# Optimization experiments

Hardware: AMD Instinct MI355X
Metric: run time of the kernel (lower is better)

## Reference

```python
import jax, jax.numpy as jnp
import numpy as np
from jax import lax

B, L, H = 2, 4096, 2048
NH = 16
DK = H // NH  # num_slot = 128 (q/k dim)
C = 64        # chunk size
EPS = 1e-5
N_LAYER = 24


def setup_inputs() -> dict:
    key = jax.random.key(0)
    ks = jax.random.split(key, 7)
    std = 0.02
    return {
        "hidden_states": jax.random.normal(ks[0], (B, L, H), jnp.float32),
        "Wq": jax.random.normal(ks[1], (DK, H), jnp.float32) * std,
        "Wk": jax.random.normal(ks[2], (DK, H), jnp.float32) * std,
        "Wog": jax.random.normal(ks[3], (H, H), jnp.float32) * std,
        "Wig": jax.random.normal(ks[4], (H, H), jnp.float32) * std,
        "Wo": jax.random.normal(ks[5], (H, H), jnp.float32) * (std / np.sqrt(2 * N_LAYER)),
        "g_norm_w": jnp.ones((H,), jnp.float32),
    }


def _gla_chunk(q, k, v, gf):
    # q,k,gf: [b,L,dk]; v: [b,L,dv]. Recurrence: S_t = diag(exp(gf_t)) S_{t-1} + k_t v_t^T; o_t = q_t S_t
    b, Ls, dk = q.shape
    dv = v.shape[-1]
    n = Ls // C
    # [n, b, C, d] so scan iterates over chunks
    qc = q.reshape(b, n, C, dk).transpose(1, 0, 2, 3)
    kc = k.reshape(b, n, C, dk).transpose(1, 0, 2, 3)
    vc = v.reshape(b, n, C, dv).transpose(1, 0, 2, 3)
    gc = gf.reshape(b, n, C, dk).transpose(1, 0, 2, 3)
    Bc = jnp.cumsum(gc, axis=2)  # inclusive within-chunk log-decay

    tril = jnp.tril(jnp.ones((C, C), bool))

    def step(S, inp):
        qh, kh, vh, Bh = inp  # [b,C,dk],[b,C,dk],[b,C,dv],[b,C,dk]
        Blast = Bh[:, -1, :]  # [b,dk]
        # exp(B_i - B_j) <= 1 for j <= i (gf < 0): numerically safe pairwise form
        D = Bh[:, :, None, :] - Bh[:, None, :, :]  # [b,C,C,dk]
        A = jnp.einsum('bid,bjd,bijd->bij', qh, kh, jnp.exp(D))
        A = jnp.where(tril, A, 0.0)
        o_intra = jnp.einsum('bij,bjv->biv', A, vh)
        o_inter = jnp.einsum('bid,bdv->biv', qh * jnp.exp(Bh), S)
        kd = kh * jnp.exp(Blast[:, None, :] - Bh)  # <= 1 scaling, safe
        S_new = S * jnp.exp(Blast)[..., None] + jnp.einsum('bjd,bjv->bdv', kd, vh)
        return S_new, o_intra + o_inter

    S0 = jnp.zeros((b, dk, dv), q.dtype)
    _, o = lax.scan(step, S0, (qc, kc, vc, Bc))  # o: [n,b,C,dv]
    return o.transpose(1, 0, 2, 3).reshape(b, Ls, dv)


def reference(hidden_states, Wq, Wk, Wog, Wig, Wo, g_norm_w):
    x = hidden_states
    q = jax.nn.softmax(x @ Wq.T, axis=-1)        # [b,L,dk]
    k = jax.nn.sigmoid(x @ Wk.T)                 # [b,L,dk]
    v = x                                        # value_dim == hidden_size
    gf = jax.nn.log_sigmoid(-k)                  # per-key-dim log decay, in (-1.32, -0.69)
    o = _gla_chunk(q, k, v, gf)                  # [b,L,H]
    # output gate: og_proj(o) + ig_proj(x), fused RMSNorm + swish gate
    go = o @ Wog.T + x @ Wig.T
    on = o * lax.rsqrt(jnp.mean(o * o, axis=-1, keepdims=True) + EPS) * g_norm_w
    o = on * (go * jax.nn.sigmoid(go))
    return o @ Wo.T
```

## Files before the change

kernel.cpp:

```cpp
#include <hip/hip_runtime.h>
#include <hip/hip_bf16.h>

typedef __hip_bfloat16 bf16;
typedef __bf16 bf16x8 __attribute__((ext_vector_type(8)));
typedef float f32x4 __attribute__((ext_vector_type(4)));

__device__ __forceinline__ void async16(void* lds_base, const void* g) {
  __builtin_amdgcn_global_load_lds(
      (const __attribute__((address_space(1))) void*)g,
      (__attribute__((address_space(3))) void*)lds_base, 16, 0, 0);
}

__global__ void cvt_bf16_kernel(const float* __restrict__ s, bf16* __restrict__ d, int n4) {
  const int i = blockIdx.x * 256 + threadIdx.x;
  if (i >= n4) return;
  const float4 v = ((const float4*)s)[i];
  bf16 h0 = __float2bfloat16(v.x), h1 = __float2bfloat16(v.y);
  bf16 h2 = __float2bfloat16(v.z), h3 = __float2bfloat16(v.w);
  ushort4 o;
  o.x = *(unsigned short*)&h0; o.y = *(unsigned short*)&h1;
  o.z = *(unsigned short*)&h2; o.w = *(unsigned short*)&h3;
  *(ushort4*)((unsigned short*)d + (size_t)i * 4) = o;
}

__global__ __launch_bounds__(256) void convert_x_kernel(
    const float* __restrict__ x, bf16* __restrict__ xb, bf16* __restrict__ xbT) {
  __shared__ float tile[64][65];
  const int b = blockIdx.z;
  const int l0 = blockIdx.x * 64, d0 = blockIdx.y * 64;
  const int t = threadIdx.x;
  const int c = t & 63, r4 = t >> 6;
  const size_t base = ((size_t)b * 4096 + l0) * 2048 + d0;
#pragma unroll
  for (int i = 0; i < 16; ++i) {
    const int row = i * 4 + r4;
    const float v = x[base + (size_t)row * 2048 + c];
    tile[row][c] = v;
    xb[base + (size_t)row * 2048 + c] = __float2bfloat16(v);
  }
  __syncthreads();
  const size_t baseT = ((size_t)b * 2048 + d0) * 4096 + l0;
#pragma unroll
  for (int i = 0; i < 16; ++i) {
    const int dr = i * 4 + r4;
    xbT[baseT + (size_t)dr * 4096 + c] = __float2bfloat16(tile[c][dr]);
  }
}

template <int MODE>
__global__ __launch_bounds__(256, 2) void gemm_bt(
    const bf16* __restrict__ A0, const bf16* __restrict__ B0,
    const bf16* __restrict__ A1, const bf16* __restrict__ B1,
    float* __restrict__ outf, bf16* __restrict__ outb,
    const bf16* __restrict__ o_in, const float* __restrict__ rmsv,
    const float* __restrict__ gnw, int M, int N, int K) {
  __shared__ bf16 lA[128 * 32];
  __shared__ bf16 lB[128 * 32];
  const int tid = threadIdx.x;
  const int lane = tid & 63, wave = tid >> 6;
  const int l15 = lane & 15, l4 = lane >> 4;
  const int bm = blockIdx.x * 128, bn = blockIdx.y * 128;
  const int wm = (wave & 1) * 64, wn = (wave >> 1) * 64;
  const int srow = tid >> 2;
  const int skc = (tid & 3) * 8;

  const f32x4 fz = {0.f, 0.f, 0.f, 0.f};
  f32x4 acc[4][4];
#pragma unroll
  for (int i = 0; i < 4; ++i)
#pragma unroll
    for (int j = 0; j < 4; ++j) acc[i][j] = fz;

  bf16* lAu  = lA + wave * 512;
  bf16* lAu2 = lA + 2048 + wave * 512;
  bf16* lBu  = lB + wave * 512;
  bf16* lBu2 = lB + 2048 + wave * 512;

  const int npass = (MODE == 1) ? 2 : 1;
  for (int pass = 0; pass < npass; ++pass) {
    const bf16* Ap = (pass == 0) ? A0 : A1;
    const bf16* Bp = (pass == 0) ? B0 : B1;
    const bf16* gA0 = Ap + (size_t)(bm + srow) * K + skc;
    const bf16* gA1 = Ap + (size_t)(bm + srow + 64) * K + skc;
    const bf16* gB0 = Bp + (size_t)(bn + srow) * K + skc;
    const bf16* gB1 = Bp + (size_t)(bn + srow + 64) * K + skc;
    for (int k0 = 0; k0 < K; k0 += 32) {
      __syncthreads();
      async16(lAu, gA0 + k0);
      async16(lAu2, gA1 + k0);
      async16(lBu, gB0 + k0);
      async16(lBu2, gB1 + k0);
      __syncthreads();
      bf16x8 af[4], bfv[4];
#pragma unroll
      for (int mt = 0; mt < 4; ++mt)
        af[mt] = *(const bf16x8*)(lA + (wm + mt * 16 + l15) * 32 + l4 * 8);
#pragma unroll
      for (int nt = 0; nt < 4; ++nt)
        bfv[nt] = *(const bf16x8*)(lB + (wn + nt * 16 + l15) * 32 + l4 * 8);
#pragma unroll
      for (int mt = 0; mt < 4; ++mt)
#pragma unroll
        for (int nt = 0; nt < 4; ++nt)
          acc[mt][nt] = __builtin_amdgcn_mfma_f32_16x16x32_bf16(af[mt], bfv[nt], acc[mt][nt], 0, 0, 0);
    }
  }

#pragma unroll
  for (int mt = 0; mt < 4; ++mt)
#pragma unroll
    for (int r = 0; r < 4; ++r) {
      const int gr = bm + wm + mt * 16 + l4 * 4 + r;
#pragma unroll
      for (int nt = 0; nt < 4; ++nt) {
        const int gc = bn + wn + nt * 16 + l15;
        const float v = acc[mt][nt][r];
        if (MODE == 1) {
          const float o = (float)o_in[(size_t)gr * N + gc];
          const float on = o * rmsv[gr] * gnw[gc];
          const float sw = v / (1.f + __expf(-v));
          outb[(size_t)gr * N + gc] = __float2bfloat16(on * sw);
        } else {
          outf[(size_t)gr * N + gc] = v;
        }
      }
    }
}

__global__ __launch_bounds__(64) void qk_post_kernel(
    const float* __restrict__ logits, bf16* __restrict__ qb,
    bf16* __restrict__ kb, float* __restrict__ gfl) {
  const int row = blockIdx.x;
  const int t = threadIdx.x;
  const float* lr = logits + (size_t)row * 256;
  float a0 = lr[t], a1 = lr[t + 64];
  float m = fmaxf(a0, a1);
#pragma unroll
  for (int s = 32; s; s >>= 1) m = fmaxf(m, __shfl_xor(m, s));
  float e0 = __expf(a0 - m), e1 = __expf(a1 - m);
  float sum = e0 + e1;
#pragma unroll
  for (int s = 32; s; s >>= 1) sum += __shfl_xor(sum, s);
  const float inv = 1.f / sum;
  qb[(size_t)row * 128 + t]      = __float2bfloat16(e0 * inv);
  qb[(size_t)row * 128 + t + 64] = __float2bfloat16(e1 * inv);
  float b0 = lr[128 + t], b1 = lr[128 + t + 64];
  float k0 = 1.f / (1.f + __expf(-b0));
  float k1 = 1.f / (1.f + __expf(-b1));
  kb[(size_t)row * 128 + t]      = __float2bfloat16(k0);
  kb[(size_t)row * 128 + t + 64] = __float2bfloat16(k1);
  gfl[(size_t)row * 128 + t]      = -log1pf(__expf(k0));
  gfl[(size_t)row * 128 + t + 64] = -log1pf(__expf(k1));
}

__global__ __launch_bounds__(256, 2) void gla_kernel(
    const bf16* __restrict__ qb, const bf16* __restrict__ kb,
    const float* __restrict__ gfl, const bf16* __restrict__ xbT,
    bf16* __restrict__ ob, float* __restrict__ rmsv) {
  __shared__ bf16 sF1[64][136];
  __shared__ bf16 sF2[128][136];
  __shared__ float sM[128];
  __shared__ float rowsq[64];
  const int tid = threadIdx.x;
  const int lane = tid & 63, wave = tid >> 6;
  const int l15 = lane & 15, l4 = lane >> 4;
  const int chunk = blockIdx.x, b = blockIdx.y;
  const int row0 = b * 4096 + chunk * 64;

  if (tid < 64) rowsq[tid] = 0.f;

  if (tid < 128) {
    float s = 0.f;
    for (int i = 0; i <= 32; ++i) s += gfl[(size_t)(row0 + i) * 128 + tid];
    sM[tid] = s;
  }
  __syncthreads();

  if (tid < 128) {
    const int d = tid;
    const float M = sM[d];
    float bi = 0.f;
    for (int i = 0; i < 64; ++i) {
      bi += gfl[(size_t)(row0 + i) * 128 + d];
      const float q = (float)qb[(size_t)(row0 + i) * 128 + d];
      const float k = (float)kb[(size_t)(row0 + i) * 128 + d];
      sF1[i][d]      = __float2bfloat16(q * __expf(bi - M));
      sF2[64 + i][d] = __float2bfloat16(k * __expf(M - bi));
    }
  } else {
    const int d = tid - 128;
    if (chunk == 0) {
      for (int j = 0; j < 64; ++j) sF2[j][d] = __float2bfloat16(0.f);
    } else {
      const float M = sM[d];
      float bw = 0.f;
      for (int j = 63; j >= 0; --j) {
        const float k = (float)kb[(size_t)(row0 - 64 + j) * 128 + d];
        sF2[j][d] = __float2bfloat16(k * __expf(M - bw));
        bw -= gfl[(size_t)(row0 - 64 + j) * 128 + d];
      }
    }
  }
  __syncthreads();

  const f32x4 fz = {0.f, 0.f, 0.f, 0.f};
  {
    f32x4 sacc[4][2];
#pragma unroll
    for (int mt = 0; mt < 4; ++mt) { sacc[mt][0] = fz; sacc[mt][1] = fz; }
    bf16x8 f1[4][4];
#pragma unroll
    for (int kt = 0; kt < 4; ++kt)
#pragma unroll
      for (int mt = 0; mt < 4; ++mt)
        f1[kt][mt] = *(const bf16x8*)(&sF1[mt * 16 + l15][kt * 32 + l4 * 8]);
#pragma unroll
    for (int nt = 0; nt < 2; ++nt)
#pragma unroll
      for (int kt = 0; kt < 4; ++kt) {
        const bf16x8 f2 = *(const bf16x8*)(&sF2[wave * 32 + nt * 16 + l15][kt * 32 + l4 * 8]);
#pragma unroll
        for (int mt = 0; mt < 4; ++mt)
          sacc[mt][nt] = __builtin_amdgcn_mfma_f32_16x16x32_bf16(f1[kt][mt], f2, sacc[mt][nt], 0, 0, 0);
      }
    __syncthreads();
#pragma unroll
    for (int mt = 0; mt < 4; ++mt)
#pragma unroll
      for (int nt = 0; nt < 2; ++nt)
#pragma unroll
        for (int r = 0; r < 4; ++r) {
          const int i = mt * 16 + l4 * 4 + r;
          const int jw = wave * 32 + nt * 16 + l15;
          const bool ok = (jw < 64) || (jw - 64 <= i);
          sF1[i][jw] = __float2bfloat16(ok ? sacc[mt][nt][r] : 0.f);
        }
    __syncthreads();
  }

  bf16x8 av[4][4];
#pragma unroll
  for (int kt = 0; kt < 4; ++kt)
#pragma unroll
    for (int mt = 0; mt < 4; ++mt)
      av[kt][mt] = *(const bf16x8*)(&sF1[mt * 16 + l15][kt * 32 + l4 * 8]);

  float rs[4][4];
#pragma unroll
  for (int a = 0; a < 4; ++a)
#pragma unroll
    for (int r2 = 0; r2 < 4; ++r2) rs[a][r2] = 0.f;

  const int lwb = chunk * 64 - 64;
  for (int dt = 0; dt < 8; ++dt) {
    const int c0 = dt * 256 + wave * 64;
    f32x4 oacc[4][4];
#pragma unroll
    for (int mt = 0; mt < 4; ++mt)
#pragma unroll
      for (int nt = 0; nt < 4; ++nt) oacc[mt][nt] = fz;
#pragma unroll
    for (int kt = 0; kt < 4; ++kt)
#pragma unroll
      for (int nt = 0; nt < 4; ++nt) {
        const int dv = c0 + nt * 16 + l15;
        int lw = lwb + kt * 32 + l4 * 8;
        if (lw < 0) lw = 0;
        const bf16x8 vv = *(const bf16x8*)(xbT + ((size_t)b * 2048 + dv) * 4096 + lw);
#pragma unroll
        for (int mt = 0; mt < 4; ++mt)
          oacc[mt][nt] = __builtin_amdgcn_mfma_f32_16x16x32_bf16(av[kt][mt], vv, oacc[mt][nt], 0, 0, 0);
      }
#pragma unroll
    for (int mt = 0; mt < 4; ++mt)
#pragma unroll
      for (int r = 0; r < 4; ++r) {
        const int i = mt * 16 + l4 * 4 + r;
#pragma unroll
        for (int nt = 0; nt < 4; ++nt) {
          const float v = oacc[mt][nt][r];
          ob[(size_t)(row0 + i) * 2048 + (c0 + nt * 16 + l15)] = __float2bfloat16(v);
          rs[mt][r] += v * v;
        }
      }
  }

#pragma unroll
  for (int mt = 0; mt < 4; ++mt)
#pragma unroll
    for (int r = 0; r < 4; ++r) {
      float v = rs[mt][r];
      v += __shfl_xor(v, 1); v += __shfl_xor(v, 2);
      v += __shfl_xor(v, 4); v += __shfl_xor(v, 8);
      if (l15 == 0) atomicAdd(&rowsq[mt * 16 + l4 * 4 + r], v);
    }
  __syncthreads();
  if (tid < 64)
    rmsv[row0 + tid] = rsqrtf(rowsq[tid] * (1.f / 2048.f) + 1e-5f);
}

extern "C" void kernel_launch(void* const* d_in, const int* in_sizes, int n_in,
                              void* d_out, int out_size, void* d_ws, size_t ws_size,
                              hipStream_t stream) {
  const float* x   = (const float*)d_in[0];
  const float* Wq  = (const float*)d_in[1];
  const float* Wk  = (const float*)d_in[2];
  const float* Wog = (const float*)d_in[3];
  const float* Wig = (const float*)d_in[4];
  const float* Wo  = (const float*)d_in[5];
  const float* gnw = (const float*)d_in[6];
  float* out = (float*)d_out;

  char* w = (char*)d_ws;
  auto alloc = [&](size_t bytes) {
    char* p = w;
    w += (bytes + 255) & ~(size_t)255;
    return p;
  };
  bf16*  wqkb   = (bf16*)alloc((size_t)256 * 2048 * 2);
  bf16*  wogb   = (bf16*)alloc((size_t)2048 * 2048 * 2);
  bf16*  wigb   = (bf16*)alloc((size_t)2048 * 2048 * 2);
  bf16*  wob    = (bf16*)alloc((size_t)2048 * 2048 * 2);
  bf16*  xb     = (bf16*)alloc((size_t)8192 * 2048 * 2);
  bf16*  xbT    = (bf16*)alloc((size_t)8192 * 2048 * 2);
  float* logits = (float*)alloc((size_t)8192 * 256 * 4);
  bf16*  qbuf   = (bf16*)alloc((size_t)8192 * 128 * 2);
  bf16*  kbuf   = (bf16*)alloc((size_t)8192 * 128 * 2);
  float* gfbuf  = (float*)alloc((size_t)8192 * 128 * 4);
  bf16*  obuf   = (bf16*)alloc((size_t)8192 * 2048 * 2);
  float* rmsbuf = (float*)alloc((size_t)8192 * 4);
  bf16*  gatedb = xbT;

  cvt_bf16_kernel<<<dim3((65536 + 255) / 256), 256, 0, stream>>>(Wq, wqkb, 65536);
  cvt_bf16_kernel<<<dim3((65536 + 255) / 256), 256, 0, stream>>>(Wk, wqkb + 262144, 65536);
  cvt_bf16_kernel<<<dim3((1048576 + 255) / 256), 256, 0, stream>>>(Wog, wogb, 1048576);
  cvt_bf16_kernel<<<dim3((1048576 + 255) / 256), 256, 0, stream>>>(Wig, wigb, 1048576);
  cvt_bf16_kernel<<<dim3((1048576 + 255) / 256), 256, 0, stream>>>(Wo, wob, 1048576);

  convert_x_kernel<<<dim3(64, 32, 2), 256, 0, stream>>>(x, xb, xbT);

  gemm_bt<0><<<dim3(64, 2), 256, 0, stream>>>(
      xb, wqkb, nullptr, nullptr, logits, nullptr, nullptr, nullptr, nullptr,
      8192, 256, 2048);

  qk_post_kernel<<<dim3(8192), 64, 0, stream>>>(logits, qbuf, kbuf, gfbuf);

  gla_kernel<<<dim3(64, 2), 256, 0, stream>>>(qbuf, kbuf, gfbuf, xbT, obuf, rmsbuf);

  gemm_bt<1><<<dim3(64, 16), 256, 0, stream>>>(
      obuf, wogb, xb, wigb, nullptr, gatedb, obuf, rmsbuf, gnw,
      8192, 2048, 2048);

  gemm_bt<2><<<dim3(64, 16), 256, 0, stream>>>(
      gatedb, wob, nullptr, nullptr, out, nullptr, nullptr, nullptr, nullptr,
      8192, 2048, 2048);

  (void)in_sizes; (void)n_in; (void)out_size; (void)ws_size;
}
```

Before: 494.6 us.

## Add 256x256-tile 8-wave GEMM with ping-pong LDS pipelining for output projections

Adds a new bf16 GEMM kernel using 256x256 output tiles, 512 threads, double-buffered LDS filled by async global-to-LDS loads, an XOR-swizzled layout, and barrier-interleaved MFMA quarters with s_setprio. It also remaps workgroup IDs across XCDs. The two large 8192x2048x2048 projection GEMMs (gated og+ig and final Wo) now use it in place of the older smaller-tile kernel. The aim is more operand reuse per LDS load and better overlap of loads with MFMA. The cost is heavy register and LDS pressure, and a fixed assumption that K is 2048.

```diff
diff --git a/kernel.cpp b/kernel.cpp
--- a/kernel.cpp
+++ b/kernel.cpp
@@ -125,6 +125,164 @@
         }
       }
     }
+}
+
+#define QMFMA(AF, BF, MH, NH)                                               \
+  do {                                                                      \
+    __builtin_amdgcn_s_setprio(1);                                          \
+    _Pragma("unroll") for (int ks_ = 0; ks_ < 2; ++ks_) {                   \
+      _Pragma("unroll") for (int mt_ = 0; mt_ < 4; ++mt_) {                 \
+        _Pragma("unroll") for (int nt_ = 0; nt_ < 2; ++nt_)                 \
+            acc[(MH) * 4 + mt_][(NH) * 2 + nt_] =                           \
+                __builtin_amdgcn_mfma_f32_16x16x32_bf16(                    \
+                    AF[mt_][ks_], BF[nt_][ks_],                             \
+                    acc[(MH) * 4 + mt_][(NH) * 2 + nt_], 0, 0, 0);          \
+      }                                                                     \
+    }                                                                       \
+    __builtin_amdgcn_s_setprio(0);                                          \
+  } while (0)
+
+template <int MODE>
+__global__ __launch_bounds__(512, 2) void gemm256(
+    const bf16* __restrict__ A0, const bf16* __restrict__ B0,
+    const bf16* __restrict__ A1, const bf16* __restrict__ B1,
+    float* __restrict__ outf, bf16* __restrict__ outb,
+    const bf16* __restrict__ o_in, const float* __restrict__ rmsv,
+    const float* __restrict__ gnw, int M, int N) {
+  __shared__ bf16 lA[2][16384];
+  __shared__ bf16 lB[2][16384];
+  const int tid = threadIdx.x;
+  const int lane = tid & 63;
+  const int wave = tid >> 6;
+  const int wmi = wave >> 2;
+  const int wni = wave & 3;
+  const int l15 = lane & 15, l4 = lane >> 4;
+  const int axor = l15 & 7;
+
+  const int nwg = gridDim.x;
+  const int cpx = nwg >> 3;
+  int wg = blockIdx.x;
+  wg = (wg & 7) * cpx + (wg >> 3);
+  const int NBN = N >> 8;
+  const int bm = (wg / NBN) * 256;
+  const int bn = (wg % NBN) * 256;
+
+  const int srow = tid >> 3;
+  const int scol = ((tid & 7) ^ (srow & 7)) * 8;
+  const size_t goff = (size_t)srow * 2048 + scol;
+
+  const int NT = (MODE == 1) ? 64 : 32;
+
+  const bf16* Abase0 = A0 + (size_t)bm * 2048;
+  const bf16* Abase1 = (MODE == 1) ? (A1 + (size_t)bm * 2048) : A0;
+  const bf16* Bbase0 = B0 + (size_t)bn * 2048;
+  const bf16* Bbase1 = (MODE == 1) ? (B1 + (size_t)bn * 2048) : B0;
+
+  auto stageA = [&](int kt, int h, int buf) {
+    int t = (kt < NT) ? kt : (NT - 1);
+    const bf16* src = Abase0;
+    int k0 = t * 64;
+    if (MODE == 1 && t >= 32) { src = Abase1; k0 = (t - 32) * 64; }
+    const bf16* g = src + (size_t)h * 128 * 2048 + k0 + goff;
+    bf16* d = &lA[buf][h * 8192] + tid * 8;
+    async16(d, g);
+    async16(d + 4096, g + (size_t)64 * 2048);
+  };
+  auto stageB = [&](int kt, int h, int buf) {
+    int t = (kt < NT) ? kt : (NT - 1);
+    const bf16* src = Bbase0;
+    int k0 = t * 64;
+    if (MODE == 1 && t >= 32) { src = Bbase1; k0 = (t - 32) * 64; }
+    const bf16* g = src + (size_t)h * 128 * 2048 + k0 + goff;
+    bf16* d = &lB[buf][h * 8192] + tid * 8;
+    async16(d, g);
+    async16(d + 4096, g + (size_t)64 * 2048);
+  };
+
+  auto readA = [&](bf16x8 (&af)[4][2], int buf, int mh) {
+    const bf16* base = &lA[buf][wmi * 8192];
+#pragma unroll
+    for (int mt = 0; mt < 4; ++mt)
+#pragma unroll
+      for (int ks = 0; ks < 2; ++ks)
+        af[mt][ks] = *(const bf16x8*)(base + (mh * 64 + mt * 16 + l15) * 64 +
+                                      (((ks * 4 + l4) ^ axor) << 3));
+  };
+  auto readB = [&](bf16x8 (&bb)[2][2], int buf, int nh) {
+    const bf16* base = &lB[buf][(wni >> 1) * 8192];
+#pragma unroll
+    for (int nt = 0; nt < 2; ++nt)
+#pragma unroll
+      for (int ks = 0; ks < 2; ++ks)
+        bb[nt][ks] = *(const bf16x8*)(base +
+                                      ((wni & 1) * 64 + nh * 32 + nt * 16 + l15) * 64 +
+                                      (((ks * 4 + l4) ^ axor) << 3));
+  };
+
+  const f32x4 fz = {0.f, 0.f, 0.f, 0.f};
+  f32x4 acc[8][4];
+#pragma unroll
+  for (int i = 0; i < 8; ++i)
+#pragma unroll
+    for (int j = 0; j < 4; ++j) acc[i][j] = fz;
+
+  stageB(0, 0, 0); stageB(0, 1, 0);
+  stageA(0, 0, 0); stageA(0, 1, 0);
+  stageB(1, 0, 1); stageB(1, 1, 1);
+  asm volatile("s_waitcnt vmcnt(4)" ::: "memory");
+  __builtin_amdgcn_s_barrier();
+
+  bf16x8 aF[4][2], b0F[2][2], b1F[2][2];
+
+  for (int kt = 0; kt < NT; ++kt) {
+    const int cur = kt & 1, nxt = cur ^ 1;
+    readA(aF, cur, 0);
+    readB(b0F, cur, 0);
+    stageA(kt + 1, 0, nxt);
+    __builtin_amdgcn_s_barrier();
+    asm volatile("s_waitcnt lgkmcnt(0)" ::: "memory");
+    QMFMA(aF, b0F, 0, 0);
+    __builtin_amdgcn_s_barrier();
+    readB(b1F, cur, 1);
+    stageA(kt + 1, 1, nxt);
+    __builtin_amdgcn_s_barrier();
+    asm volatile("s_waitcnt lgkmcnt(0)" ::: "memory");
+    QMFMA(aF, b1F, 0, 1);
+    __builtin_amdgcn_s_barrier();
+    readA(aF, cur, 1);
+    stageB(kt + 2, 0, cur);
+    __builtin_amdgcn_s_barrier();
+    asm volatile("s_waitcnt lgkmcnt(0)" ::: "memory");
+    QMFMA(aF, b0F, 1, 0);
+    __builtin_amdgcn_s_barrier();
+    stageB(kt + 2, 1, cur);
+    asm volatile("s_waitcnt vmcnt(4)" ::: "memory");
+    __builtin_amdgcn_s_barrier();
+    QMFMA(aF, b1F, 1, 1);
+    __builtin_amdgcn_s_barrier();
+    __builtin_amdgcn_sched_barrier(0);
+  }
+
+#pragma unroll
+  for (int i = 0; i < 8; ++i) {
+#pragma unroll
+    for (int r = 0; r < 4; ++r) {
+      const int gr = bm + wmi * 128 + i * 16 + l4 * 4 + r;
+#pragma unroll
+      for (int j = 0; j < 4; ++j) {
+        const int gc = bn + wni * 64 + j * 16 + l15;
+        const float v = acc[i][j][r];
+        if (MODE == 1) {
+          const float o = (float)o_in[(size_t)gr * N + gc];
+          const float on = o * rmsv[gr] * gnw[gc];
+          const float sw = v / (1.f + __expf(-v));
+          outb[(size_t)gr * N + gc] = __float2bfloat16(on * sw);
+        } else {
+          outf[(size_t)gr * N + gc] = v;
+        }
+      }
+    }
+  }
 }
 
 __global__ __launch_bounds__(64) void qk_post_kernel(
@@ -347,13 +505,12 @@
 
   gla_kernel<<<dim3(64, 2), 256, 0, stream>>>(qbuf, kbuf, gfbuf, xbT, obuf, rmsbuf);
 
-  gemm_bt<1><<<dim3(64, 16), 256, 0, stream>>>(
-      obuf, wogb, xb, wigb, nullptr, gatedb, obuf, rmsbuf, gnw,
-      8192, 2048, 2048);
-
-  gemm_bt<2><<<dim3(64, 16), 256, 0, stream>>>(
+  gemm256<1><<<dim3(256), 512, 0, stream>>>(
+      obuf, wogb, xb, wigb, nullptr, gatedb, obuf, rmsbuf, gnw, 8192, 2048);
+
+  gemm256<2><<<dim3(256), 512, 0, stream>>>(
       gatedb, wob, nullptr, nullptr, out, nullptr, nullptr, nullptr, nullptr,
-      8192, 2048, 2048);
+      8192, 2048);
 
   (void)in_sizes; (void)n_in; (void)out_size; (void)ws_size;
 }
```

New measurement: 469.0 us. 1.05x faster.
